# Optimization experiments

Hardware: AMD Instinct MI355X
Metric: run time of the kernel (lower is better)

## Reference

```python
import jax, jax.numpy as jnp
import numpy as np
from jax import lax

N = 2048
P = 256
F_J = 0.05      # sparsity of recurrent matrix J
F_OUT = 0.05    # sparsity of readout
DT = 0.1
ON_TIME = 10
T = 200


def _activation(x):
    # Tanh_shifted_and_scaled: rates in [0, 1]
    return 0.5 * (1.0 + jnp.tanh(x))


def setup_inputs() -> dict:
    key = jax.random.key(0)
    k1, k2, k3, k4, k5 = jax.random.split(key, 5)
    # patterns ~ Uniform(-1, 1), shape [N, P]
    patterns = jax.random.uniform(k1, (N, P), jnp.float32, -1.0, 1.0)
    # sparse recurrent matrix J: gaussian values, density F_J, gain g
    g = 10.0 * 0.1 ** 0.25 / np.sqrt(N * P * np.sqrt(F_J))
    J_dense = jax.random.normal(k2, (N, N), jnp.float32) * jnp.float32(g)
    mask = jax.random.uniform(k3, (N, N)) < F_J
    J = jnp.where(mask, J_dense, 0.0).astype(jnp.float32)
    # sparse readout: ones at a random F_OUT fraction of units (frozen)
    w_out = (jax.random.uniform(k4, (N,)) < F_OUT).astype(jnp.float32)
    return {"patterns": patterns, "J": J, "w_out": w_out, "N_time_steps": T}


def reference(patterns, J, w_out, N_time_steps):
    # Batched over all P patterns at once (columns of [N, P] state).
    n = patterns.shape[0]
    x0 = jnp.zeros_like(patterns)           # [N, P]
    r0 = _activation(x0)

    def step(carry, ti):
        x, rates = carry
        inp = jnp.where(ti < ON_TIME, patterns, 0.0)      # [N, P]
        x = x + DT * (-x + J @ rates + inp)               # [N, P]
        rates = _activation(x)
        out_t = w_out @ rates                             # [P]
        return (x, rates), out_t

    _, outs = lax.scan(step, (x0, r0), jnp.arange(N_time_steps))  # [T, P]
    readout = outs.T / n                                   # [P, T]
    return readout
```

## Files before the change

### kernel.cpp

```cpp
#include <hip/hip_runtime.h>
#include <hip/hip_bf16.h>


#define NN 2048
#define PP 256
#define DT_C 0.1f
#define ON_TIME_C 10

typedef __attribute__((ext_vector_type(8))) short bf16x8;
typedef __attribute__((ext_vector_type(4))) float f32x4;

__device__ __forceinline__ unsigned short bf16rne(float f) {
    unsigned b = __float_as_uint(f);
    return (unsigned short)((b + 0x7FFFu + ((b >> 16) & 1u)) >> 16);
}
__device__ __forceinline__ int kperm(int s) {
    return ((s & 15) >> 2) * 8 + (s & 3) + ((s >> 4) << 2);
}

__global__ void convert_J_kernel(const float* __restrict__ J,
                                 unsigned short* __restrict__ Jp) {
    int i = blockIdx.x * blockDim.x + threadIdx.x;
    int row = i >> 11, k = i & 2047;
    Jp[((size_t)row << 11) + (k & ~31) + kperm(k & 31)] = bf16rne(J[i]);
}

__global__ void init_kernel(float* __restrict__ x,
                            unsigned short* __restrict__ rT,
                            float* __restrict__ out, int nout) {
    int i = blockIdx.x * blockDim.x + threadIdx.x;
    x[i] = 0.0f;
    rT[i] = 0x3F00;
    if (i < nout) out[i] = 0.0f;
}

#define AS1 __attribute__((address_space(1)))
#define AS3 __attribute__((address_space(3)))
#define GLOAD16(g, l) \
    __builtin_amdgcn_global_load_lds((const AS1 void*)(g), (AS3 void*)(l), 16, 0, 0)

__global__ __launch_bounds__(512, 1) void gemm_step_kernel(
    const unsigned short* __restrict__ Jp,
    const unsigned short* __restrict__ rin,
    unsigned short* __restrict__ rout,
    float* __restrict__ x, const float* __restrict__ patterns,
    const float* __restrict__ w_out, float* __restrict__ out,
    int t, int T, int with_input) {

    __shared__ char smem[98304];

    const int tid  = threadIdx.x;
    const int w    = tid >> 6;
    const int lane = tid & 63;
    const int wm   = w >> 1, wn = w & 1;

    const int bid   = (blockIdx.x & 7) * 32 + (blockIdx.x >> 3);
    const int mbase = (bid >> 3) * 64;
    const int nbase = (bid & 7) * 32;

    const int rA0 = 8 * w + (lane >> 4);
    const int rA1 = rA0 + 4;
    const int rB  = 4 * w + (lane >> 4);
    const char* gA0 = (const char*)Jp  + (((size_t)(mbase + rA0)) << 12)
                      + (((lane & 15) ^ (rA0 & 15)) << 4);
    const char* gA1 = (const char*)Jp  + (((size_t)(mbase + rA1)) << 12)
                      + (((lane & 15) ^ (rA1 & 15)) << 4);
    const char* gB  = (const char*)rin + (((size_t)(nbase + rB )) << 12)
                      + (((lane & 15) ^ (rB  & 15)) << 4);
    const int ldsA0 = (8 * w)     * 256;
    const int ldsA1 = (8 * w + 4) * 256;
    const int ldsB  = 16384 + 4 * w * 256;

    const int mr = wm * 16 + (lane & 15);
    const int nr = wn * 16 + (lane & 15);

    float xv[4], pat[4], wsc[4];
    #pragma unroll
    for (int rg = 0; rg < 4; ++rg) {
        int m = mbase + wm * 16 + (lane >> 4) * 4 + rg;
        int n = nbase + wn * 16 + (lane & 15);
        size_t o = ((size_t)m << 8) + n;
        xv[rg]  = x[o];
        pat[rg] = with_input ? patterns[o] : 0.0f;
        wsc[rg] = (w_out[m] != 0.0f) ? (1.0f / (float)NN) : 0.0f;
    }

    f32x4 acc = {0.f, 0.f, 0.f, 0.f};

    GLOAD16(gA0,       smem + 0 * 24576 + ldsA0);
    GLOAD16(gA1,       smem + 0 * 24576 + ldsA1);
    GLOAD16(gB,        smem + 0 * 24576 + ldsB);
    GLOAD16(gA0 + 256, smem + 1 * 24576 + ldsA0);
    GLOAD16(gA1 + 256, smem + 1 * 24576 + ldsA1);
    GLOAD16(gB  + 256, smem + 1 * 24576 + ldsB);

    #pragma unroll
    for (int ph = 0; ph < 16; ++ph) {
        if (ph < 14) {
            const int bo = ((ph + 2) & 3) * 24576;
            GLOAD16(gA0 + (ph + 2) * 256, smem + bo + ldsA0);
            GLOAD16(gA1 + (ph + 2) * 256, smem + bo + ldsA1);
            GLOAD16(gB  + (ph + 2) * 256, smem + bo + ldsB);
        }
        if (ph < 14)       asm volatile("s_waitcnt vmcnt(6)" ::: "memory");
        else if (ph == 14) asm volatile("s_waitcnt vmcnt(3)" ::: "memory");
        else               asm volatile("s_waitcnt vmcnt(0)" ::: "memory");
        __builtin_amdgcn_s_barrier();
        __builtin_amdgcn_sched_barrier(0);

        const int bb = (ph & 3) * 24576;
        bf16x8 a[4], b[4];
        #pragma unroll
        for (int g = 0; g < 4; ++g) {
            int c = g * 4 + (lane >> 4);
            a[g] = *(const bf16x8*)(smem + bb + mr * 256 + ((c ^ (mr & 15)) << 4));
            b[g] = *(const bf16x8*)(smem + bb + 16384 + nr * 256 + ((c ^ (nr & 15)) << 4));
        }
        #pragma unroll
        for (int g = 0; g < 4; ++g)
            acc = __builtin_amdgcn_mfma_f32_16x16x32_bf16(a[g], b[g], acc, 0, 0, 0);
    }

    __syncthreads();

    #pragma unroll
    for (int rg = 0; rg < 4; ++rg) {
        float xo = xv[rg];
        float xn = xo + DT_C * (acc[rg] + pat[rg] - xo);
        int mloc = wm * 16 + (lane >> 4) * 4 + rg;
        int nloc = wn * 16 + (lane & 15);
        int m = mbase + mloc, n = nbase + nloc;
        x[((size_t)m << 8) + n] = xn;
        float r = 0.5f * (1.0f + tanhf(xn));
        if (wsc[rg] != 0.0f)
            atomicAdd(&out[(size_t)n * T + t], r * wsc[rg]);
        int pos  = (mloc & ~31) + kperm(mloc & 31);
        int byte = nloc * 128 + (((pos >> 3) ^ (nloc & 7)) << 4) + (pos & 7) * 2;
        *(unsigned short*)(smem + byte) = bf16rne(r);
    }
    __syncthreads();
    if (tid < 256) {
        int nl = tid >> 3, p = tid & 7;
        uint4 v = *(const uint4*)(smem + nl * 128 + ((p ^ (nl & 7)) << 4));
        *(uint4*)((char*)rout + (((size_t)(nbase + nl)) << 12) + mbase * 2 + p * 16) = v;
    }
}

extern "C" void kernel_launch(void* const* d_in, const int* in_sizes, int n_in,
                              void* d_out, int out_size, void* d_ws, size_t ws_size,
                              hipStream_t stream) {
    const float* patterns = (const float*)d_in[0];
    const float* J        = (const float*)d_in[1];
    const float* w_out    = (const float*)d_in[2];
    float* out            = (float*)d_out;

    int T = out_size / PP;

    size_t off = 0;
    auto alloc = [&](size_t bytes) {
        void* p = (char*)d_ws + off;
        off += (bytes + 255) & ~(size_t)255;
        return p;
    };
    unsigned short* Jp = (unsigned short*)alloc((size_t)NN * NN * 2);
    unsigned short* r0 = (unsigned short*)alloc((size_t)PP * NN * 2);
    unsigned short* r1 = (unsigned short*)alloc((size_t)PP * NN * 2);
    float*          x  = (float*)         alloc((size_t)NN * PP * 4);
    (void)ws_size; (void)n_in; (void)in_sizes;

    convert_J_kernel<<<(NN * NN) / 256, 256, 0, stream>>>(J, Jp);
    init_kernel<<<(NN * PP) / 256, 256, 0, stream>>>(x, r0, out, PP * T);

    for (int t = 0; t < T; ++t) {
        const unsigned short* rin = (t & 1) ? r1 : r0;
        unsigned short*      rout = (t & 1) ? r0 : r1;
        gemm_step_kernel<<<256, 512, 0, stream>>>(Jp, rin, rout, x, patterns,
                                                  w_out, out, t, T,
                                                  (t < ON_TIME_C) ? 1 : 0);
    }
}
```

Measured before the change: 1.972 ms.

## Fuse all time steps into one persistent cooperative kernel with grid barrier

Replaces the per-timestep launch loop with a single cooperative persistent kernel. It keeps x in registers across steps and synchronises blocks through an atomic counter grid barrier between steps. B loads use a different cache-policy bit. This removes the overhead of 200 kernel launches and the x global round trip, at the cost of a spin barrier per step. The old multi-launch path stays as a fallback.

```diff
diff --git a/kernel.cpp b/kernel.cpp
--- a/kernel.cpp
+++ b/kernel.cpp
@@ -27,25 +27,27 @@
 
 __global__ void init_kernel(float* __restrict__ x,
                             unsigned short* __restrict__ rT,
-                            float* __restrict__ out, int nout) {
+                            float* __restrict__ out, int nout,
+                            unsigned* __restrict__ cnt) {
     int i = blockIdx.x * blockDim.x + threadIdx.x;
     x[i] = 0.0f;
     rT[i] = 0x3F00;
     if (i < nout) out[i] = 0.0f;
+    if (i == 0) *cnt = 0u;
 }
 
 #define AS1 __attribute__((address_space(1)))
 #define AS3 __attribute__((address_space(3)))
-#define GLOAD16(g, l) \
+#define GLOADA(g, l) \
     __builtin_amdgcn_global_load_lds((const AS1 void*)(g), (AS3 void*)(l), 16, 0, 0)
-
-__global__ __launch_bounds__(512, 1) void gemm_step_kernel(
+#define GLOADB(g, l) \
+    __builtin_amdgcn_global_load_lds((const AS1 void*)(g), (AS3 void*)(l), 16, 0, 16)
+
+__global__ __launch_bounds__(512, 1) void srnn_persist(
     const unsigned short* __restrict__ Jp,
-    const unsigned short* __restrict__ rin,
-    unsigned short* __restrict__ rout,
-    float* __restrict__ x, const float* __restrict__ patterns,
-    const float* __restrict__ w_out, float* __restrict__ out,
-    int t, int T, int with_input) {
+    unsigned short* __restrict__ r0, unsigned short* __restrict__ r1,
+    const float* __restrict__ patterns, const float* __restrict__ w_out,
+    float* __restrict__ out, unsigned* __restrict__ cnt, int T) {
 
     __shared__ char smem[98304];
 
@@ -54,6 +56,127 @@
     const int lane = tid & 63;
     const int wm   = w >> 1, wn = w & 1;
 
+    const int bid   = (blockIdx.x & 7) * 32 + (blockIdx.x >> 3);
+    const int mbase = (bid >> 3) * 64;
+    const int nbase = (bid & 7) * 32;
+
+    const int rA0 = 8 * w + (lane >> 4);
+    const int rA1 = rA0 + 4;
+    const int rB  = 4 * w + (lane >> 4);
+    const char* gA0 = (const char*)Jp + (((size_t)(mbase + rA0)) << 12)
+                      + (((lane & 15) ^ (rA0 & 15)) << 4);
+    const char* gA1 = (const char*)Jp + (((size_t)(mbase + rA1)) << 12)
+                      + (((lane & 15) ^ (rA1 & 15)) << 4);
+    const size_t gBoff = (((size_t)(nbase + rB)) << 12)
+                      + (((lane & 15) ^ (rB & 15)) << 4);
+    const int ldsA0 = (8 * w) * 256, ldsA1 = (8 * w + 4) * 256;
+    const int ldsB  = 16384 + 4 * w * 256;
+
+    const int mr = wm * 16 + (lane & 15);
+    const int nr = wn * 16 + (lane & 15);
+    const int nloc = wn * 16 + (lane & 15);
+    const int n    = nbase + nloc;
+
+    float xv[4], pat[4], wsc[4];
+    #pragma unroll
+    for (int rg = 0; rg < 4; ++rg) {
+        int m = mbase + wm * 16 + (lane >> 4) * 4 + rg;
+        size_t o = ((size_t)m << 8) + n;
+        xv[rg]  = 0.0f;
+        pat[rg] = patterns[o];
+        wsc[rg] = (w_out[m] != 0.0f) ? (1.0f / (float)NN) : 0.0f;
+    }
+
+    for (int t = 0; t < T; ++t) {
+        const char* rbas = (t & 1) ? (const char*)r1 : (const char*)r0;
+        char*       robs = (t & 1) ? (char*)r0 : (char*)r1;
+        const char* gB   = rbas + gBoff;
+
+        GLOADA(gA0,       smem + 0 * 24576 + ldsA0);
+        GLOADA(gA1,       smem + 0 * 24576 + ldsA1);
+        GLOADB(gB,        smem + 0 * 24576 + ldsB);
+        GLOADA(gA0 + 256, smem + 1 * 24576 + ldsA0);
+        GLOADA(gA1 + 256, smem + 1 * 24576 + ldsA1);
+        GLOADB(gB  + 256, smem + 1 * 24576 + ldsB);
+
+        f32x4 acc = {0.f, 0.f, 0.f, 0.f};
+
+        #pragma unroll
+        for (int ph = 0; ph < 16; ++ph) {
+            if (ph < 14) {
+                const int bo = ((ph + 2) & 3) * 24576;
+                GLOADA(gA0 + (ph + 2) * 256, smem + bo + ldsA0);
+                GLOADA(gA1 + (ph + 2) * 256, smem + bo + ldsA1);
+                GLOADB(gB  + (ph + 2) * 256, smem + bo + ldsB);
+            }
+            if (ph < 14)       asm volatile("s_waitcnt vmcnt(6)" ::: "memory");
+            else if (ph == 14) asm volatile("s_waitcnt vmcnt(3)" ::: "memory");
+            else               asm volatile("s_waitcnt vmcnt(0)" ::: "memory");
+            __builtin_amdgcn_s_barrier();
+            __builtin_amdgcn_sched_barrier(0);
+
+            const int bb = (ph & 3) * 24576;
+            bf16x8 a[4], b[4];
+            #pragma unroll
+            for (int g = 0; g < 4; ++g) {
+                int c = g * 4 + (lane >> 4);
+                a[g] = *(const bf16x8*)(smem + bb + mr * 256 + ((c ^ (mr & 15)) << 4));
+                b[g] = *(const bf16x8*)(smem + bb + 16384 + nr * 256 + ((c ^ (nr & 15)) << 4));
+            }
+            #pragma unroll
+            for (int g = 0; g < 4; ++g)
+                acc = __builtin_amdgcn_mfma_f32_16x16x32_bf16(a[g], b[g], acc, 0, 0, 0);
+        }
+
+        __syncthreads();
+
+        #pragma unroll
+        for (int rg = 0; rg < 4; ++rg) {
+            float xo = xv[rg];
+            float inp = (t < ON_TIME_C) ? pat[rg] : 0.0f;
+            float xn = xo + DT_C * (acc[rg] + inp - xo);
+            xv[rg] = xn;
+            float r = 0.5f * (1.0f + tanhf(xn));
+            if (wsc[rg] != 0.0f)
+                atomicAdd(&out[(size_t)n * T + t], r * wsc[rg]);
+            int mloc = wm * 16 + (lane >> 4) * 4 + rg;
+            int pos  = (mloc & ~31) + kperm(mloc & 31);
+            int byte = nloc * 128 + (((pos >> 3) ^ (nloc & 7)) << 4) + (pos & 7) * 2;
+            *(unsigned short*)(smem + byte) = bf16rne(r);
+        }
+        __syncthreads();
+        if (tid < 256) {
+            int nl = tid >> 3, p = tid & 7;
+            uint4 v = *(const uint4*)(smem + nl * 128 + ((p ^ (nl & 7)) << 4));
+            *(uint4*)(robs + (((size_t)(nbase + nl)) << 12) + mbase * 2 + p * 16) = v;
+        }
+        __syncthreads();
+
+        if (tid == 0) {
+            __builtin_amdgcn_fence(__ATOMIC_RELEASE, "agent");
+            __hip_atomic_fetch_add(cnt, 1u, __ATOMIC_RELAXED,
+                                   __HIP_MEMORY_SCOPE_AGENT);
+            unsigned tgt = 256u * (unsigned)(t + 1);
+            while (__hip_atomic_load(cnt, __ATOMIC_RELAXED,
+                                     __HIP_MEMORY_SCOPE_AGENT) < tgt)
+                __builtin_amdgcn_s_sleep(4);
+        }
+        __syncthreads();
+    }
+}
+
+__global__ __launch_bounds__(512, 1) void gemm_step_kernel(
+    const unsigned short* __restrict__ Jp,
+    const unsigned short* __restrict__ rin, unsigned short* __restrict__ rout,
+    float* __restrict__ x, const float* __restrict__ patterns,
+    const float* __restrict__ w_out, float* __restrict__ out,
+    int t, int T, int with_input) {
+
+    __shared__ char smem[98304];
+    const int tid  = threadIdx.x;
+    const int w    = tid >> 6;
+    const int lane = tid & 63;
+    const int wm   = w >> 1, wn = w & 1;
     const int bid   = (blockIdx.x & 7) * 32 + (blockIdx.x >> 3);
     const int mbase = (bid >> 3) * 64;
     const int nbase = (bid & 7) * 32;
@@ -67,10 +190,8 @@
                       + (((lane & 15) ^ (rA1 & 15)) << 4);
     const char* gB  = (const char*)rin + (((size_t)(nbase + rB )) << 12)
                       + (((lane & 15) ^ (rB  & 15)) << 4);
-    const int ldsA0 = (8 * w)     * 256;
-    const int ldsA1 = (8 * w + 4) * 256;
+    const int ldsA0 = (8 * w) * 256, ldsA1 = (8 * w + 4) * 256;
     const int ldsB  = 16384 + 4 * w * 256;
-
     const int mr = wm * 16 + (lane & 15);
     const int nr = wn * 16 + (lane & 15);
 
@@ -86,21 +207,20 @@
     }
 
     f32x4 acc = {0.f, 0.f, 0.f, 0.f};
-
-    GLOAD16(gA0,       smem + 0 * 24576 + ldsA0);
-    GLOAD16(gA1,       smem + 0 * 24576 + ldsA1);
-    GLOAD16(gB,        smem + 0 * 24576 + ldsB);
-    GLOAD16(gA0 + 256, smem + 1 * 24576 + ldsA0);
-    GLOAD16(gA1 + 256, smem + 1 * 24576 + ldsA1);
-    GLOAD16(gB  + 256, smem + 1 * 24576 + ldsB);
+    GLOADA(gA0,       smem + 0 * 24576 + ldsA0);
+    GLOADA(gA1,       smem + 0 * 24576 + ldsA1);
+    GLOADA(gB,        smem + 0 * 24576 + ldsB);
+    GLOADA(gA0 + 256, smem + 1 * 24576 + ldsA0);
+    GLOADA(gA1 + 256, smem + 1 * 24576 + ldsA1);
+    GLOADA(gB  + 256, smem + 1 * 24576 + ldsB);
 
     #pragma unroll
     for (int ph = 0; ph < 16; ++ph) {
         if (ph < 14) {
             const int bo = ((ph + 2) & 3) * 24576;
-            GLOAD16(gA0 + (ph + 2) * 256, smem + bo + ldsA0);
-            GLOAD16(gA1 + (ph + 2) * 256, smem + bo + ldsA1);
-            GLOAD16(gB  + (ph + 2) * 256, smem + bo + ldsB);
+            GLOADA(gA0 + (ph + 2) * 256, smem + bo + ldsA0);
+            GLOADA(gA1 + (ph + 2) * 256, smem + bo + ldsA1);
+            GLOADA(gB  + (ph + 2) * 256, smem + bo + ldsB);
         }
         if (ph < 14)       asm volatile("s_waitcnt vmcnt(6)" ::: "memory");
         else if (ph == 14) asm volatile("s_waitcnt vmcnt(3)" ::: "memory");
@@ -122,7 +242,6 @@
     }
 
     __syncthreads();
-
     #pragma unroll
     for (int rg = 0; rg < 4; ++rg) {
         float xo = xv[rg];
@@ -162,14 +281,26 @@
         off += (bytes + 255) & ~(size_t)255;
         return p;
     };
-    unsigned short* Jp = (unsigned short*)alloc((size_t)NN * NN * 2);
-    unsigned short* r0 = (unsigned short*)alloc((size_t)PP * NN * 2);
-    unsigned short* r1 = (unsigned short*)alloc((size_t)PP * NN * 2);
-    float*          x  = (float*)         alloc((size_t)NN * PP * 4);
+    unsigned short* Jp  = (unsigned short*)alloc((size_t)NN * NN * 2);
+    unsigned short* r0  = (unsigned short*)alloc((size_t)PP * NN * 2);
+    unsigned short* r1  = (unsigned short*)alloc((size_t)PP * NN * 2);
+    float*          x   = (float*)         alloc((size_t)NN * PP * 4);
+    unsigned*       cnt = (unsigned*)      alloc(256);
     (void)ws_size; (void)n_in; (void)in_sizes;
 
     convert_J_kernel<<<(NN * NN) / 256, 256, 0, stream>>>(J, Jp);
-    init_kernel<<<(NN * PP) / 256, 256, 0, stream>>>(x, r0, out, PP * T);
+    init_kernel<<<(NN * PP) / 256, 256, 0, stream>>>(x, r0, out, PP * T, cnt);
+
+    int mb = 0;
+    if (hipOccupancyMaxActiveBlocksPerMultiprocessor(
+            &mb, (const void*)srnn_persist, 512, 0) == hipSuccess && mb >= 1) {
+        void* args[] = {(void*)&Jp, (void*)&r0, (void*)&r1, (void*)&patterns,
+                        (void*)&w_out, (void*)&out, (void*)&cnt, (void*)&T};
+        if (hipLaunchCooperativeKernel((const void*)srnn_persist,
+                                       dim3(256), dim3(512), args, 0,
+                                       stream) == hipSuccess)
+            return;
+    }
 
     for (int t = 0; t < T; ++t) {
         const unsigned short* rin = (t & 1) ? r1 : r0;
```

Result: no change. 1.978 ms (+0.3%).

## Use 32x32x16 MFMA with split-K across waves and LDS reduction

Applied to the files above, without the earlier changes.

Replaces the per-wave 16x16x32 MFMA tiling with 32x32x16 MFMAs, where each wave covers a 32x32 sub-tile over one quarter of each K chunk. The four partial sums are then reduced through LDS. The J repacking permutation changes to match the new K-lane layout, and the epilogue switches to float4 loads and stores of x and patterns. This is meant to issue fewer MFMA instructions and LDS fragment reads per step and to vectorize the epilogue, at the cost of an extra LDS round trip and a reduction across waves.

```diff
diff --git a/kernel.cpp b/kernel.cpp
--- a/kernel.cpp
+++ b/kernel.cpp
@@ -7,22 +7,22 @@
 #define DT_C 0.1f
 #define ON_TIME_C 10
 
-typedef __attribute__((ext_vector_type(8))) short bf16x8;
-typedef __attribute__((ext_vector_type(4))) float f32x4;
+typedef __attribute__((ext_vector_type(8)))  short bf16x8;
+typedef __attribute__((ext_vector_type(16))) float f32x16;
 
 __device__ __forceinline__ unsigned short bf16rne(float f) {
     unsigned b = __float_as_uint(f);
     return (unsigned short)((b + 0x7FFFu + ((b >> 16) & 1u)) >> 16);
 }
-__device__ __forceinline__ int kperm(int s) {
-    return ((s & 15) >> 2) * 8 + (s & 3) + ((s >> 4) << 2);
+__device__ __forceinline__ int kperm16(int s) {
+    return (s & 3) + (((s >> 2) & 1) << 3) + ((s >> 3) << 2);
 }
 
 __global__ void convert_J_kernel(const float* __restrict__ J,
                                  unsigned short* __restrict__ Jp) {
     int i = blockIdx.x * blockDim.x + threadIdx.x;
     int row = i >> 11, k = i & 2047;
-    Jp[((size_t)row << 11) + (k & ~31) + kperm(k & 31)] = bf16rne(J[i]);
+    Jp[((size_t)row << 11) + (k & ~15) + kperm16(k & 15)] = bf16rne(J[i]);
 }
 
 __global__ void init_kernel(float* __restrict__ x,
@@ -52,7 +52,9 @@
     const int tid  = threadIdx.x;
     const int w    = tid >> 6;
     const int lane = tid & 63;
-    const int wm   = w >> 1, wn = w & 1;
+    const int s    = w >> 2;
+    const int kq   = w & 3;
+    const int h    = lane >> 5;
 
     const int bid   = (blockIdx.x & 7) * 32 + (blockIdx.x >> 3);
     const int mbase = (bid >> 3) * 64;
@@ -67,25 +69,13 @@
                       + (((lane & 15) ^ (rA1 & 15)) << 4);
     const char* gB  = (const char*)rin + (((size_t)(nbase + rB )) << 12)
                       + (((lane & 15) ^ (rB  & 15)) << 4);
-    const int ldsA0 = (8 * w)     * 256;
-    const int ldsA1 = (8 * w + 4) * 256;
+    const int ldsA0 = (8 * w) * 256, ldsA1 = (8 * w + 4) * 256;
     const int ldsB  = 16384 + 4 * w * 256;
 
-    const int mr = wm * 16 + (lane & 15);
-    const int nr = wn * 16 + (lane & 15);
-
-    float xv[4], pat[4], wsc[4];
-    #pragma unroll
-    for (int rg = 0; rg < 4; ++rg) {
-        int m = mbase + wm * 16 + (lane >> 4) * 4 + rg;
-        int n = nbase + wn * 16 + (lane & 15);
-        size_t o = ((size_t)m << 8) + n;
-        xv[rg]  = x[o];
-        pat[rg] = with_input ? patterns[o] : 0.0f;
-        wsc[rg] = (w_out[m] != 0.0f) ? (1.0f / (float)NN) : 0.0f;
-    }
-
-    f32x4 acc = {0.f, 0.f, 0.f, 0.f};
+    const int rA = 32 * s + (lane & 31);
+    const int rBn = lane & 31;
+
+    f32x16 acc = {};
 
     GLOAD16(gA0,       smem + 0 * 24576 + ldsA0);
     GLOAD16(gA1,       smem + 0 * 24576 + ldsA1);
@@ -109,39 +99,70 @@
         __builtin_amdgcn_sched_barrier(0);
 
         const int bb = (ph & 3) * 24576;
-        bf16x8 a[4], b[4];
         #pragma unroll
-        for (int g = 0; g < 4; ++g) {
-            int c = g * 4 + (lane >> 4);
-            a[g] = *(const bf16x8*)(smem + bb + mr * 256 + ((c ^ (mr & 15)) << 4));
-            b[g] = *(const bf16x8*)(smem + bb + 16384 + nr * 256 + ((c ^ (nr & 15)) << 4));
-        }
+        for (int sl = 0; sl < 2; ++sl) {
+            const int c = kq * 4 + sl * 2 + h;
+            bf16x8 a = *(const bf16x8*)(smem + bb + rA * 256
+                                        + ((c ^ (rA & 15)) << 4));
+            bf16x8 b = *(const bf16x8*)(smem + bb + 16384 + rBn * 256
+                                        + ((c ^ (rBn & 15)) << 4));
+            acc = __builtin_amdgcn_mfma_f32_32x32x16_bf16(a, b, acc, 0, 0, 0);
+        }
+    }
+
+    __syncthreads();
+
+    {
+        float* pf = (float*)smem;
+        const int plane = (s * 4 + kq) * 1024;
         #pragma unroll
-        for (int g = 0; g < 4; ++g)
-            acc = __builtin_amdgcn_mfma_f32_16x16x32_bf16(a[g], b[g], acc, 0, 0, 0);
-    }
-
+        for (int reg = 0; reg < 16; ++reg) {
+            int row = (reg & 3) + 8 * (reg >> 2) + 4 * h;
+            pf[plane + row * 32 + (lane & 31)] = acc[reg];
+        }
+    }
     __syncthreads();
 
-    #pragma unroll
-    for (int rg = 0; rg < 4; ++rg) {
-        float xo = xv[rg];
-        float xn = xo + DT_C * (acc[rg] + pat[rg] - xo);
-        int mloc = wm * 16 + (lane >> 4) * 4 + rg;
-        int nloc = wn * 16 + (lane & 15);
-        int m = mbase + mloc, n = nbase + nloc;
-        x[((size_t)m << 8) + n] = xn;
-        float r = 0.5f * (1.0f + tanhf(xn));
-        if (wsc[rg] != 0.0f)
-            atomicAdd(&out[(size_t)n * T + t], r * wsc[rg]);
-        int pos  = (mloc & ~31) + kperm(mloc & 31);
-        int byte = nloc * 128 + (((pos >> 3) ^ (nloc & 7)) << 4) + (pos & 7) * 2;
-        *(unsigned short*)(smem + byte) = bf16rne(r);
+    {
+        const int s2 = tid >> 8, rr = (tid >> 3) & 31, c4 = (tid & 7) * 4;
+        const float4* pf4 = (const float4*)smem;
+        int base = ((s2 * 4) * 1024 + rr * 32 + c4) >> 2;
+        float4 v0 = pf4[base], v1 = pf4[base + 256];
+        float4 v2 = pf4[base + 512], v3 = pf4[base + 768];
+        float sum[4] = {v0.x + v1.x + v2.x + v3.x, v0.y + v1.y + v2.y + v3.y,
+                        v0.z + v1.z + v2.z + v3.z, v0.w + v1.w + v2.w + v3.w};
+
+        const int mloc = s2 * 32 + rr;
+        const int m = mbase + mloc;
+        const int n0 = nbase + c4;
+        size_t xo = ((size_t)m << 8) + n0;
+        float4 xv = *(const float4*)(x + xo);
+        float4 pv = make_float4(0.f, 0.f, 0.f, 0.f);
+        if (with_input) pv = *(const float4*)(patterns + xo);
+        float wsc = (w_out[m] != 0.0f) ? (1.0f / (float)NN) : 0.0f;
+
+        float xn[4] = {xv.x + DT_C * (sum[0] + pv.x - xv.x),
+                       xv.y + DT_C * (sum[1] + pv.y - xv.y),
+                       xv.z + DT_C * (sum[2] + pv.z - xv.z),
+                       xv.w + DT_C * (sum[3] + pv.w - xv.w)};
+        *(float4*)(x + xo) = make_float4(xn[0], xn[1], xn[2], xn[3]);
+
+        const int pos = (mloc & ~15) + kperm16(mloc & 15);
+        #pragma unroll
+        for (int j = 0; j < 4; ++j) {
+            float r = 0.5f * (1.0f + tanhf(xn[j]));
+            if (wsc != 0.0f)
+                atomicAdd(&out[(size_t)(n0 + j) * T + t], r * wsc);
+            int nloc = c4 + j;
+            int byte = 32768 + nloc * 128
+                     + (((pos >> 3) ^ (nloc & 7)) << 4) + (pos & 7) * 2;
+            *(unsigned short*)(smem + byte) = bf16rne(r);
+        }
     }
     __syncthreads();
     if (tid < 256) {
         int nl = tid >> 3, p = tid & 7;
-        uint4 v = *(const uint4*)(smem + nl * 128 + ((p ^ (nl & 7)) << 4));
+        uint4 v = *(const uint4*)(smem + 32768 + nl * 128 + ((p ^ (nl & 7)) << 4));
         *(uint4*)((char*)rout + (((size_t)(nbase + nl)) << 12) + mbase * 2 + p * 16) = v;
     }
 }
```

Result: faster. 1.932 ms (-2.1%).
